# Kernel tuning notes

Measured on AMD Instinct MI355X. Metric: run time of the kernel, lower is better.

The kernel has to match this reference:

```python
import jax, jax.numpy as jnp
import numpy as np

# Edge-type order matches edge_types dict: (src-out i, src-in j)
_ET = ((0, 0), (0, 1), (1, 0), (1, 1))


def _gcn_multi(h0, h1, W, rows, cols, vals, N):
    """One heterogeneous GraphConvolutionMulti pass.

    For each edge type t=(i,j): out_i += adj_t @ (h_j @ W[t]), where adj_t is
    sparse [N,N] given as (rows[t], cols[t], vals[t]).
    Returns pre-activation outputs [out0, out1], each [N, dout].
    """
    hs = (h0, h1)
    dout = W.shape[2]
    outs = [jnp.zeros((N, dout), h0.dtype), jnp.zeros((N, dout), h0.dtype)]
    for t, (i, j) in enumerate(_ET):
        hw = hs[j] @ W[t]                      # [N, dout] dense GEMM
        msg = vals[t][:, None] * hw[cols[t]]   # [E, dout] gather
        outs[i] = outs[i] + jax.ops.segment_sum(msg, rows[t], num_segments=N)
    return outs


def setup_inputs() -> dict:
    key = jax.random.key(0)
    ks = jax.random.split(key, 12)
    N, F, H, E = 100000, 128, 64, 1000000
    inp = {
        "feat0": jax.random.normal(ks[0], (N, F), jnp.float32),
        "feat1": jax.random.normal(ks[1], (N, F), jnp.float32),
        "rows": jax.random.randint(ks[2], (4, E), 0, N, jnp.int32),
        "cols": jax.random.randint(ks[3], (4, E), 0, N, jnp.int32),
        # small positive values ~ normalized adjacency weights
        "vals": jax.random.uniform(ks[4], (4, E), jnp.float32) * 0.05,
        "W1": jax.random.normal(ks[5], (4, F, H), jnp.float32) * 0.05,
        "W2": jax.random.normal(ks[6], (4, H, H), jnp.float32) * 0.05,
        "W3": jax.random.normal(ks[7], (4, H, H), jnp.float32) * 0.05,
        "W4": jax.random.normal(ks[8], (4, H, H), jnp.float32) * 0.05,
        "W5": jax.random.normal(ks[9], (4, H, H), jnp.float32) * 0.05,
        "att": jnp.array([0.9, 0.45, 0.4, 0.3, 0.2], jnp.float32),
    }
    return inp


def reference(feat0, feat1, rows, cols, vals, W1, W2, W3, W4, W5, att):
    N = feat0.shape[0]
    relu = jax.nn.relu
    # layer 1 (sparse-feature conv): hidden1[i] = relu(sum_j adj_ij @ feat_j W)
    a = _gcn_multi(feat0, feat1, W1, rows, cols, vals, N)
    h1 = [relu(a[0]), relu(a[1])]
    # layers 2-4: hidden2->hidden2 convs with relu(add_n)
    a = _gcn_multi(h1[0], h1[1], W2, rows, cols, vals, N)
    e1 = [relu(a[0]), relu(a[1])]
    a = _gcn_multi(e1[0], e1[1], W3, rows, cols, vals, N)
    e2 = [relu(a[0]), relu(a[1])]
    a = _gcn_multi(e2[0], e2[1], W4, rows, cols, vals, N)
    e3 = [relu(a[0]), relu(a[1])]
    # layer 5: embeddings = add_n(reltyp4) (NO relu) + hidden1 residual
    p = _gcn_multi(e3[0], e3[1], W5, rows, cols, vals, N)
    emb = [p[0] + h1[0], p[1] + h1[1]]
    # attention-weighted concat of depth-1, depth-2 and final embeddings
    f0 = jnp.concatenate([h1[0] * att[0], e1[0] * att[1], emb[0] * att[2]], axis=1)
    f1 = jnp.concatenate([h1[1] * att[0], e1[1] * att[1], emb[1] * att[2]], axis=1)
    return jnp.stack([f0, f1])  # [2, N, 3*H]
```

## Files before the change

kernel.cpp:

```cpp
#include <hip/hip_runtime.h>
#include <hip/hip_fp16.h>


#define HDIM 64

__device__ inline unsigned pack2h(float a, float b) {
    return (unsigned)__half_as_ushort(__float2half_rn(a)) |
           ((unsigned)__half_as_ushort(__float2half_rn(b)) << 16);
}

__global__ __launch_bounds__(256) void gemm_l1(const float* __restrict__ in0,
                                               const float* __restrict__ in1,
                                               const float* __restrict__ Wall,
                                               __half* __restrict__ hw16, int N) {
    const int K = 128;
    __shared__ __align__(16) float Ws[128 * 64];
    __shared__ __align__(16) float As[16 * 68];

    const int t = blockIdx.y;
    const float* A = (t & 1) ? in1 : in0;
    const float* W = Wall + (size_t)t * K * HDIM;
    __half*      C = hw16 + (size_t)t * (size_t)N * HDIM;

    const int tid  = threadIdx.x;
    const int row0 = blockIdx.x * 64;

    for (int off = tid * 4; off < K * 64; off += 1024)
        *(float4*)(Ws + off) = *(const float4*)(W + off);

    const int tx = tid & 15;
    const int ty = tid >> 4;
    const int lr = tid >> 2;
    const int kq = tid & 3;

    float acc[4][4];
#pragma unroll
    for (int i = 0; i < 4; i++)
#pragma unroll
        for (int j = 0; j < 4; j++) acc[i][j] = 0.f;

    const int grow = row0 + lr;
    const float* Arow = A + (size_t)grow * K;

    for (int k0 = 0; k0 < K; k0 += 16) {
        __syncthreads();
        float4 av = make_float4(0.f, 0.f, 0.f, 0.f);
        if (grow < N) av = *(const float4*)(Arow + k0 + kq * 4);
        As[(kq * 4 + 0) * 68 + lr] = av.x;
        As[(kq * 4 + 1) * 68 + lr] = av.y;
        As[(kq * 4 + 2) * 68 + lr] = av.z;
        As[(kq * 4 + 3) * 68 + lr] = av.w;
        __syncthreads();

#pragma unroll
        for (int kk = 0; kk < 16; kk++) {
            float4 a4 = *(const float4*)(As + kk * 68 + ty * 4);
            float4 b4 = *(const float4*)(Ws + (k0 + kk) * 64 + tx * 4);
            float avv[4] = {a4.x, a4.y, a4.z, a4.w};
            float bvv[4] = {b4.x, b4.y, b4.z, b4.w};
#pragma unroll
            for (int i = 0; i < 4; i++)
#pragma unroll
                for (int j = 0; j < 4; j++)
                    acc[i][j] = fmaf(avv[i], bvv[j], acc[i][j]);
        }
    }

#pragma unroll
    for (int i = 0; i < 4; i++) {
        int r = row0 + ty * 4 + i;
        if (r < N) {
            uint2 pk;
            pk.x = pack2h(acc[i][0], acc[i][1]);
            pk.y = pack2h(acc[i][2], acc[i][3]);
            *(uint2*)(C + (size_t)r * HDIM + tx * 4) = pk;
        }
    }
}

template <int MODE>
__global__ __launch_bounds__(256) void gemm_h2(const float* __restrict__ g,
                                               const float* __restrict__ Wl,
                                               __half* __restrict__ o16,
                                               float* __restrict__ o32,
                                               const float* __restrict__ h1,
                                               const float* __restrict__ e1,
                                               const float* __restrict__ att,
                                               float* __restrict__ outF, int N) {
    const int K = 128;
    __shared__ __align__(16) float Ws[128 * 64];
    __shared__ __align__(16) float As[16 * 68];

    const int t = blockIdx.y;
    const size_t NH = (size_t)N * HDIM;
    const float* A = g + (size_t)t * (size_t)N * K;
    const float* W = Wl + (size_t)t * 8192;

    const int tid  = threadIdx.x;
    const int row0 = blockIdx.x * 64;

    for (int off = tid * 4; off < K * 64; off += 1024)
        *(float4*)(Ws + off) = *(const float4*)(W + off);

    const int tx = tid & 15;
    const int ty = tid >> 4;
    const int lr = tid >> 2;
    const int kq = tid & 3;

    float acc[4][4];
#pragma unroll
    for (int i = 0; i < 4; i++)
#pragma unroll
        for (int j = 0; j < 4; j++) acc[i][j] = 0.f;

    const int grow = row0 + lr;
    const float* Arow = A + (size_t)grow * K;

    for (int k0 = 0; k0 < K; k0 += 16) {
        __syncthreads();
        float4 av = make_float4(0.f, 0.f, 0.f, 0.f);
        if (grow < N) av = *(const float4*)(Arow + k0 + kq * 4);
        As[(kq * 4 + 0) * 68 + lr] = av.x;
        As[(kq * 4 + 1) * 68 + lr] = av.y;
        As[(kq * 4 + 2) * 68 + lr] = av.z;
        As[(kq * 4 + 3) * 68 + lr] = av.w;
        __syncthreads();

#pragma unroll
        for (int kk = 0; kk < 16; kk++) {
            float4 a4 = *(const float4*)(As + kk * 68 + ty * 4);
            float4 b4 = *(const float4*)(Ws + (k0 + kk) * 64 + tx * 4);
            float avv[4] = {a4.x, a4.y, a4.z, a4.w};
            float bvv[4] = {b4.x, b4.y, b4.z, b4.w};
#pragma unroll
            for (int i = 0; i < 4; i++)
#pragma unroll
                for (int j = 0; j < 4; j++)
                    acc[i][j] = fmaf(avv[i], bvv[j], acc[i][j]);
        }
    }

    if (MODE != 2) {
#pragma unroll
        for (int i = 0; i < 4; i++) {
            int r = row0 + ty * 4 + i;
            if (r < N) {
                size_t idx = (size_t)t * NH + (size_t)r * HDIM + tx * 4;
                uint2 pk;
                pk.x = pack2h(acc[i][0], acc[i][1]);
                pk.y = pack2h(acc[i][2], acc[i][3]);
                *(uint2*)(o16 + idx) = pk;
                if (MODE == 1) {
                    float4 o = make_float4(acc[i][0], acc[i][1], acc[i][2], acc[i][3]);
                    *(float4*)(o32 + idx) = o;
                }
            }
        }
    } else {
        const float a0 = att[0], a1 = att[1], a2 = att[2];
#pragma unroll
        for (int i = 0; i < 4; i++) {
            int r = row0 + ty * 4 + i;
            if (r < N) {
                size_t idx = (size_t)t * NH + (size_t)r * HDIM + tx * 4;
                float4 h4 = *(const float4*)(h1 + idx);
                float4 e4 = *(const float4*)(e1 + idx);
                float hh[4] = {fmaxf(h4.x, 0.f), fmaxf(h4.y, 0.f),
                               fmaxf(h4.z, 0.f), fmaxf(h4.w, 0.f)};
                float ee[4] = {fmaxf(e4.x, 0.f), fmaxf(e4.y, 0.f),
                               fmaxf(e4.z, 0.f), fmaxf(e4.w, 0.f)};
                size_t base = (size_t)t * (size_t)N * 192 + (size_t)r * 192 + tx * 4;
                *(float4*)(outF + base) =
                    make_float4(hh[0] * a0, hh[1] * a0, hh[2] * a0, hh[3] * a0);
                *(float4*)(outF + base + 64) =
                    make_float4(ee[0] * a1, ee[1] * a1, ee[2] * a1, ee[3] * a1);
                *(float4*)(outF + base + 128) =
                    make_float4((acc[i][0] + hh[0]) * a2, (acc[i][1] + hh[1]) * a2,
                                (acc[i][2] + hh[2]) * a2, (acc[i][3] + hh[3]) * a2);
            }
        }
    }
}


__global__ __launch_bounds__(256) void hist4(const int* __restrict__ rows,
                                             int* __restrict__ cnt, int E, int N) {
    int e = blockIdx.x * 256 + threadIdx.x;
    int t = blockIdx.y;
    if (e < E) atomicAdd(&cnt[t * N + rows[(size_t)t * E + e]], 1);
}

__global__ __launch_bounds__(256) void scan_sums(const int* __restrict__ cnt,
                                                 int* __restrict__ partials, int M) {
    __shared__ int red[256];
    int base = blockIdx.x * 1024 + threadIdx.x * 4;
    int s = 0;
#pragma unroll
    for (int j = 0; j < 4; j++) {
        int i = base + j;
        if (i < M) s += (cnt[i] + 7) & ~7;
    }
    red[threadIdx.x] = s;
    __syncthreads();
    for (int off = 128; off > 0; off >>= 1) {
        if (threadIdx.x < off) red[threadIdx.x] += red[threadIdx.x + off];
        __syncthreads();
    }
    if (threadIdx.x == 0) partials[blockIdx.x] = red[0];
}

__global__ __launch_bounds__(1024) void scan_partials(int* __restrict__ partials, int B) {
    __shared__ int buf[1024];
    int t = threadIdx.x;
    int v = (t < B) ? partials[t] : 0;
    buf[t] = v;
    __syncthreads();
    for (int off = 1; off < 1024; off <<= 1) {
        int add = (t >= off) ? buf[t - off] : 0;
        __syncthreads();
        buf[t] += add;
        __syncthreads();
    }
    if (t < B) partials[t] = buf[t] - v;
}

__global__ __launch_bounds__(256) void scan_final(int* __restrict__ cnt,
                                                  const int* __restrict__ partials,
                                                  int* __restrict__ start, int M) {
    __shared__ int red[256];
    int tid = threadIdx.x;
    int base = blockIdx.x * 1024 + tid * 4;
    int v[4];
    int s = 0;
#pragma unroll
    for (int j = 0; j < 4; j++) {
        int i = base + j;
        v[j] = (i < M) ? ((cnt[i] + 7) & ~7) : 0;
        s += v[j];
    }
    red[tid] = s;
    __syncthreads();
    int mine = s;
    for (int off = 1; off < 256; off <<= 1) {
        int add = (tid >= off) ? red[tid - off] : 0;
        __syncthreads();
        red[tid] += add;
        __syncthreads();
    }
    int excl = red[tid] - mine + partials[blockIdx.x];
#pragma unroll
    for (int j = 0; j < 4; j++) {
        int i = base + j;
        if (i < M) {
            start[i] = excl;
            cnt[i]   = excl;
            excl += v[j];
            if (i == M - 1) start[M] = excl;
        }
    }
}

__global__ __launch_bounds__(256) void reorder4(const int* __restrict__ rows,
                                                const int* __restrict__ cols,
                                                const float* __restrict__ vals,
                                                int* __restrict__ cursor,
                                                int2* __restrict__ spair,
                                                int E, int N) {
    int e = blockIdx.x * 256 + threadIdx.x;
    int t = blockIdx.y;
    if (e >= E) return;
    size_t o = (size_t)t * E + e;
    int pos = atomicAdd(&cursor[t * N + rows[o]], 1);
    spair[pos] = make_int2(cols[o], __float_as_int(vals[o]));
}


__global__ __launch_bounds__(256) void gatherA(const __half* __restrict__ hw16,
                                               const int* __restrict__ start,
                                               const int4* __restrict__ sp4,
                                               float* __restrict__ h32,
                                               __half* __restrict__ h16, int N) {
    const int half = blockIdx.y;
    const int row  = blockIdx.x * 4 + (threadIdx.x >> 6);
    const int lane = threadIdx.x & 63;
    if (row >= N) return;
    const size_t NH = (size_t)N * HDIM;
    float accA = 0.f, accB = 0.f;

#pragma unroll
    for (int p = 0; p < 2; p++) {
        const int tt = half * 2 + p;
        const __half* __restrict__ h = hw16 + (size_t)tt * NH;
        int beg = __builtin_amdgcn_readfirstlane(start[tt * N + row]);
        int end = __builtin_amdgcn_readfirstlane(start[tt * N + row + 1]);
        for (int e = beg; e < end; e += 8) {
            int c[8]; float v[8];
#pragma unroll
            for (int u = 0; u < 4; u++) {
                int4 q = sp4[(e >> 1) + u];
                c[2 * u]     = q.x; v[2 * u]     = __int_as_float(q.y);
                c[2 * u + 1] = q.z; v[2 * u + 1] = __int_as_float(q.w);
            }
            float hv[8];
#pragma unroll
            for (int u = 0; u < 8; u++)
                hv[u] = __half2float(h[(size_t)c[u] * HDIM + lane]);
#pragma unroll
            for (int u = 0; u < 8; u += 2) {
                accA = fmaf(v[u],     hv[u],     accA);
                accB = fmaf(v[u + 1], hv[u + 1], accB);
            }
        }
    }
    float r = accA + accB;
    size_t idx = (size_t)half * NH + (size_t)row * HDIM + lane;
    h32[idx] = r;
    h16[idx] = __float2half_rn(r);
}

__global__ __launch_bounds__(256) void gatherF(const __half* __restrict__ in16,
                                               const int* __restrict__ start,
                                               const int4* __restrict__ sp4,
                                               float* __restrict__ g, int N) {
    const int half = blockIdx.y;
    const int row  = blockIdx.x * 4 + (threadIdx.x >> 6);
    const int lane = threadIdx.x & 63;
    if (row >= N) return;
    const size_t NH = (size_t)N * HDIM;
    float* gout = g + ((size_t)half * N + row) * 128 + lane;

#pragma unroll
    for (int p = 0; p < 2; p++) {
        const int tt = half * 2 + p;
        const __half* __restrict__ h = in16 + (size_t)(tt & 1) * NH;
        int beg = __builtin_amdgcn_readfirstlane(start[tt * N + row]);
        int end = __builtin_amdgcn_readfirstlane(start[tt * N + row + 1]);
        float accA = 0.f, accB = 0.f;
        for (int e = beg; e < end; e += 8) {
            int c[8]; float v[8];
#pragma unroll
            for (int u = 0; u < 4; u++) {
                int4 q = sp4[(e >> 1) + u];
                c[2 * u]     = q.x; v[2 * u]     = __int_as_float(q.y);
                c[2 * u + 1] = q.z; v[2 * u + 1] = __int_as_float(q.w);
            }
            float hv[8];
#pragma unroll
            for (int u = 0; u < 8; u++)
                hv[u] = fmaxf(__half2float(h[(size_t)c[u] * HDIM + lane]), 0.f);
#pragma unroll
            for (int u = 0; u < 8; u += 2) {
                accA = fmaf(v[u],     hv[u],     accA);
                accB = fmaf(v[u + 1], hv[u + 1], accB);
            }
        }
        gout[p * 64] = accA + accB;
    }
}

extern "C" void kernel_launch(void* const* d_in, const int* in_sizes, int n_in,
                              void* d_out, int out_size, void* d_ws, size_t ws_size,
                              hipStream_t stream) {
    const float* feat0 = (const float*)d_in[0];
    const float* feat1 = (const float*)d_in[1];
    const int*   rows  = (const int*)d_in[2];
    const int*   cols  = (const int*)d_in[3];
    const float* vals  = (const float*)d_in[4];
    const float* W1    = (const float*)d_in[5];
    const float* W2    = (const float*)d_in[6];
    const float* W3    = (const float*)d_in[7];
    const float* W4    = (const float*)d_in[8];
    const float* W5    = (const float*)d_in[9];
    const float* att   = (const float*)d_in[10];

    const int N = in_sizes[0] / 128;
    const int E = in_sizes[2] / 4;
    const size_t NH = (size_t)N * HDIM;
    const int M = 4 * N;
    const int PadCap = 4 * E + 7 * M;

    float* ws  = (float*)d_ws;
    float* h10 = ws + 0 * NH;
    float* e10 = ws + 2 * NH;
    float* g   = ws + 4 * NH;
    __half* hw16 = (__half*)g;
    __half* f16  = (__half*)(ws + 8 * NH);
    __half* h16  = f16 + 0 * 2 * NH;
    __half* e16  = f16 + 1 * 2 * NH;
    __half* a16  = f16 + 2 * 2 * NH;
    __half* b16  = f16 + 3 * 2 * NH;

    int2*  spair    = (int2*)(ws + 12 * NH);
    int*   start    = (int*)(spair + PadCap);
    int*   cursor   = start + (M + 1);
    int*   partials = cursor + M;

    const int gblk = (N + 63) / 64;
    const int eblk = (E + 255) / 256;
    const int B    = (M + 1023) / 1024;
    const int gr2  = (N + 3) / 4;

    hipMemsetAsync(cursor, 0, (size_t)M * sizeof(int), stream);
    hipMemsetAsync(spair, 0, (size_t)PadCap * sizeof(int2), stream);
    hist4<<<dim3(eblk, 4), 256, 0, stream>>>(rows, cursor, E, N);
    scan_sums<<<B, 256, 0, stream>>>(cursor, partials, M);
    scan_partials<<<1, 1024, 0, stream>>>(partials, B);
    scan_final<<<B, 256, 0, stream>>>(cursor, partials, start, M);
    reorder4<<<dim3(eblk, 4), 256, 0, stream>>>(rows, cols, vals, cursor, spair, E, N);

    const int4* sp4 = (const int4*)spair;

    gemm_l1<<<dim3(gblk, 4), 256, 0, stream>>>(feat0, feat1, W1, hw16, N);
    gatherA<<<dim3(gr2, 2), 256, 0, stream>>>(hw16, start, sp4, h10, h16, N);

    gatherF<<<dim3(gr2, 2), 256, 0, stream>>>(h16, start, sp4, g, N);
    gemm_h2<1><<<dim3(gblk, 2), 256, 0, stream>>>(g, W2, e16, e10,
                                                  nullptr, nullptr, nullptr, nullptr, N);

    gatherF<<<dim3(gr2, 2), 256, 0, stream>>>(e16, start, sp4, g, N);
    gemm_h2<0><<<dim3(gblk, 2), 256, 0, stream>>>(g, W3, a16, nullptr,
                                                  nullptr, nullptr, nullptr, nullptr, N);
    gatherF<<<dim3(gr2, 2), 256, 0, stream>>>(a16, start, sp4, g, N);
    gemm_h2<0><<<dim3(gblk, 2), 256, 0, stream>>>(g, W4, b16, nullptr,
                                                  nullptr, nullptr, nullptr, nullptr, N);

    gatherF<<<dim3(gr2, 2), 256, 0, stream>>>(b16, start, sp4, g, N);
    gemm_h2<2><<<dim3(gblk, 2), 256, 0, stream>>>(g, W5, nullptr, nullptr,
                                                  h10, e10, att, (float*)d_out, N);
}
```

Measured before the change: 1.471 ms.

## Split CSR reorder scatter into two-pass binned scatter for write locality

```diff
diff --git a/kernel.cpp b/kernel.cpp
--- a/kernel.cpp
+++ b/kernel.cpp
@@ -3,6 +3,7 @@
 
 
 #define HDIM 64
+#define BINW 1680
 
 __device__ inline unsigned pack2h(float a, float b) {
     return (unsigned)__half_as_ushort(__float2half_rn(a)) |
@@ -260,18 +261,36 @@
     }
 }
 
-__global__ __launch_bounds__(256) void reorder4(const int* __restrict__ rows,
-                                                const int* __restrict__ cols,
-                                                const float* __restrict__ vals,
-                                                int* __restrict__ cursor,
-                                                int2* __restrict__ spair,
-                                                int E, int N) {
+__global__ __launch_bounds__(256) void scatter_bins(const int* __restrict__ rows,
+                                                    const int* __restrict__ cols,
+                                                    const float* __restrict__ vals,
+                                                    int* __restrict__ cursor,
+                                                    int* __restrict__ bincnt,
+                                                    unsigned* __restrict__ binbuf,
+                                                    int E, int N) {
     int e = blockIdx.x * 256 + threadIdx.x;
     int t = blockIdx.y;
     if (e >= E) return;
     size_t o = (size_t)t * E + e;
     int pos = atomicAdd(&cursor[t * N + rows[o]], 1);
-    spair[pos] = make_int2(cols[o], __float_as_int(vals[o]));
+    int b   = pos / BINW;
+    int idx = atomicAdd(&bincnt[b], 1);
+    size_t rb = ((size_t)b * BINW + idx) * 3;
+    binbuf[rb]     = (unsigned)pos;
+    binbuf[rb + 1] = (unsigned)cols[o];
+    binbuf[rb + 2] = __float_as_uint(vals[o]);
+}
+
+__global__ __launch_bounds__(256) void place_bins(const int* __restrict__ bincnt,
+                                                  const unsigned* __restrict__ binbuf,
+                                                  int2* __restrict__ spair) {
+    int b = blockIdx.x;
+    int n = bincnt[b];
+    const unsigned* rec = binbuf + (size_t)b * BINW * 3;
+    for (int i = threadIdx.x; i < n; i += 256) {
+        unsigned pos = rec[3 * i];
+        spair[pos] = make_int2((int)rec[3 * i + 1], (int)rec[3 * i + 2]);
+    }
 }
 
 
@@ -378,12 +397,14 @@
     const size_t NH = (size_t)N * HDIM;
     const int M = 4 * N;
     const int PadCap = 4 * E + 7 * M;
+    const int NBINS  = (PadCap + BINW - 1) / BINW;
 
     float* ws  = (float*)d_ws;
     float* h10 = ws + 0 * NH;
     float* e10 = ws + 2 * NH;
     float* g   = ws + 4 * NH;
     __half* hw16 = (__half*)g;
+    unsigned* binbuf = (unsigned*)g;
     __half* f16  = (__half*)(ws + 8 * NH);
     __half* h16  = f16 + 0 * 2 * NH;
     __half* e16  = f16 + 1 * 2 * NH;
@@ -394,6 +415,7 @@
     int*   start    = (int*)(spair + PadCap);
     int*   cursor   = start + (M + 1);
     int*   partials = cursor + M;
+    int*   bincnt   = partials + 1024;
 
     const int gblk = (N + 63) / 64;
     const int eblk = (E + 255) / 256;
@@ -401,12 +423,15 @@
     const int gr2  = (N + 3) / 4;
 
     hipMemsetAsync(cursor, 0, (size_t)M * sizeof(int), stream);
+    hipMemsetAsync(bincnt, 0, (size_t)NBINS * sizeof(int), stream);
     hipMemsetAsync(spair, 0, (size_t)PadCap * sizeof(int2), stream);
     hist4<<<dim3(eblk, 4), 256, 0, stream>>>(rows, cursor, E, N);
     scan_sums<<<B, 256, 0, stream>>>(cursor, partials, M);
     scan_partials<<<1, 1024, 0, stream>>>(partials, B);
     scan_final<<<B, 256, 0, stream>>>(cursor, partials, start, M);
-    reorder4<<<dim3(eblk, 4), 256, 0, stream>>>(rows, cols, vals, cursor, spair, E, N);
+    scatter_bins<<<dim3(eblk, 4), 256, 0, stream>>>(rows, cols, vals, cursor,
+                                                    bincnt, binbuf, E, N);
+    place_bins<<<NBINS, 256, 0, stream>>>(bincnt, binbuf, spair);
 
     const int4* sp4 = (const int4*)spair;
 
```

Result: slower. 2.090 ms (+42.1%).

## Replace atomic CSR reorder with two-pass bucketed split and LDS placement

Applied to the files above, without the earlier changes.

```diff
diff --git a/kernel.cpp b/kernel.cpp
--- a/kernel.cpp
+++ b/kernel.cpp
@@ -3,6 +3,10 @@
 
 
 #define HDIM 64
+#define STRIPES 16
+#define BROWS   128
+#define RCAP    160
+#define SPANCAP 3072
 
 __device__ inline unsigned pack2h(float a, float b) {
     return (unsigned)__half_as_ushort(__float2half_rn(a)) |
@@ -253,25 +257,80 @@
         int i = base + j;
         if (i < M) {
             start[i] = excl;
-            cnt[i]   = excl;
             excl += v[j];
             if (i == M - 1) start[M] = excl;
         }
     }
 }
 
-__global__ __launch_bounds__(256) void reorder4(const int* __restrict__ rows,
-                                                const int* __restrict__ cols,
-                                                const float* __restrict__ vals,
-                                                int* __restrict__ cursor,
-                                                int2* __restrict__ spair,
-                                                int E, int N) {
-    int e = blockIdx.x * 256 + threadIdx.x;
-    int t = blockIdx.y;
-    if (e >= E) return;
-    size_t o = (size_t)t * E + e;
-    int pos = atomicAdd(&cursor[t * N + rows[o]], 1);
-    spair[pos] = make_int2(cols[o], __float_as_int(vals[o]));
+__global__ __launch_bounds__(256) void split_pass(const int* __restrict__ rows,
+                                                  const int* __restrict__ cols,
+                                                  const float* __restrict__ vals,
+                                                  int2* __restrict__ rbuf,
+                                                  int* __restrict__ cnt_sb,
+                                                  int E, int nbt) {
+    __shared__ int cur[1024];
+    const int s = blockIdx.x;
+    const int t = blockIdx.y;
+    for (int i = threadIdx.x; i < nbt; i += 256) cur[i] = 0;
+    __syncthreads();
+
+    const int es = (E + STRIPES - 1) / STRIPES;
+    const int e0 = s * es;
+    const int e1 = min(e0 + es, E);
+    const size_t base = (size_t)t * E;
+    int2* rb = rbuf + (size_t)(t * STRIPES + s) * nbt * RCAP;
+
+    for (int e = e0 + threadIdx.x; e < e1; e += 256) {
+        int r = rows[base + e];
+        int b = r >> 7;
+        int idx = atomicAdd(&cur[b], 1);
+        if (idx < RCAP) {
+            int rl = r & 127;
+            rb[(size_t)b * RCAP + idx] =
+                make_int2((rl << 17) | cols[base + e], __float_as_int(vals[base + e]));
+        }
+    }
+    __syncthreads();
+    for (int i = threadIdx.x; i < nbt; i += 256)
+        cnt_sb[(t * STRIPES + s) * nbt + i] = min(cur[i], RCAP);
+}
+
+__global__ __launch_bounds__(256) void place_pass(const int2* __restrict__ rbuf,
+                                                  const int* __restrict__ cnt_sb,
+                                                  const int* __restrict__ start,
+                                                  int2* __restrict__ spair,
+                                                  int N, int nbt) {
+    __shared__ int  lcur[BROWS];
+    __shared__ int2 span[SPANCAP];
+    const int b = blockIdx.x;
+    const int t = blockIdx.y;
+    const int r0 = b * BROWS;
+    const int rows_here = min(BROWS, N - r0);
+    if (rows_here <= 0) return;
+    const int g0 = t * N + r0;
+    const int p0 = start[g0];
+    const int p1 = start[g0 + rows_here];
+    const int spanlen = p1 - p0;
+
+    for (int i = threadIdx.x; i < spanlen; i += 256) span[i] = make_int2(0, 0);
+    for (int i = threadIdx.x; i < rows_here; i += 256) lcur[i] = start[g0 + i] - p0;
+    __syncthreads();
+
+    for (int s = 0; s < STRIPES; s++) {
+        const int sb = (t * STRIPES + s) * nbt + b;
+        const int n = cnt_sb[sb];
+        const int2* rec = rbuf + (size_t)sb * RCAP;
+        for (int i = threadIdx.x; i < n; i += 256) {
+            int2 q = rec[i];
+            int rl = ((unsigned)q.x) >> 17;
+            int idx = atomicAdd(&lcur[rl], 1);
+            if (idx < SPANCAP) span[idx] = make_int2(q.x & 0x1FFFF, q.y);
+        }
+    }
+    __syncthreads();
+    int2* out = spair + p0;
+    for (int i = threadIdx.x; i < spanlen; i += 256) out[i] = span[i];
 }
 
 
@@ -378,12 +437,14 @@
     const size_t NH = (size_t)N * HDIM;
     const int M = 4 * N;
     const int PadCap = 4 * E + 7 * M;
+    const int nbt = (N + BROWS - 1) / BROWS;
 
     float* ws  = (float*)d_ws;
     float* h10 = ws + 0 * NH;
     float* e10 = ws + 2 * NH;
     float* g   = ws + 4 * NH;
     __half* hw16 = (__half*)g;
+    int2*   rbuf = (int2*)g;
     __half* f16  = (__half*)(ws + 8 * NH);
     __half* h16  = f16 + 0 * 2 * NH;
     __half* e16  = f16 + 1 * 2 * NH;
@@ -394,6 +455,7 @@
     int*   start    = (int*)(spair + PadCap);
     int*   cursor   = start + (M + 1);
     int*   partials = cursor + M;
+    int*   cnt_sb   = partials + 1024;
 
     const int gblk = (N + 63) / 64;
     const int eblk = (E + 255) / 256;
@@ -401,12 +463,12 @@
     const int gr2  = (N + 3) / 4;
 
     hipMemsetAsync(cursor, 0, (size_t)M * sizeof(int), stream);
-    hipMemsetAsync(spair, 0, (size_t)PadCap * sizeof(int2), stream);
     hist4<<<dim3(eblk, 4), 256, 0, stream>>>(rows, cursor, E, N);
     scan_sums<<<B, 256, 0, stream>>>(cursor, partials, M);
     scan_partials<<<1, 1024, 0, stream>>>(partials, B);
     scan_final<<<B, 256, 0, stream>>>(cursor, partials, start, M);
-    reorder4<<<dim3(eblk, 4), 256, 0, stream>>>(rows, cols, vals, cursor, spair, E, N);
+    split_pass<<<dim3(STRIPES, 4), 256, 0, stream>>>(rows, cols, vals, rbuf, cnt_sb, E, nbt);
+    place_pass<<<dim3(nbt, 4), 256, 0, stream>>>(rbuf, cnt_sb, start, spair, N, nbt);
 
     const int4* sp4 = (const int4*)spair;
 
```

New measurement: 1.484 ms. Within noise of the previous version (+0.9%).
